# Optimization experiments

Hardware: AMD Instinct MI355X
Metric: run time of the kernel (lower is better)

Reference implementation:

```python
import jax, jax.numpy as jnp
import numpy as np

NUM_HEADS = 8
HEAD_DIM = 64  # inner_dim 512 / 8 heads
SCALE = HEAD_DIM ** -0.5


def setup_inputs() -> dict:
    key = jax.random.key(0)
    kq, kk, kv, kp = jax.random.split(key, 4)
    B, S, D = 8, 1024, 512
    q = jax.random.normal(kq, (B, S, D), dtype=jnp.float32)
    k = jax.random.normal(kk, (B, S, D), dtype=jnp.float32)
    v = jax.random.normal(kv, (B, S, D), dtype=jnp.float32)
    # learned additive positional bias table (trunc-normal init approximated by normal clipped)
    pos_bias = jnp.clip(jax.random.normal(kp, (1, NUM_HEADS, S, S), dtype=jnp.float32), -2.0, 2.0)
    return {"q": q, "k": k, "v": v, "pos_bias": pos_bias}


def reference(q, k, v, pos_bias):
    B, S, D = q.shape
    h, d = NUM_HEADS, HEAD_DIM
    # b n (h d) -> b h n d
    qh = q.reshape(B, S, h, d).transpose(0, 2, 1, 3) * SCALE
    kh = k.reshape(B, S, h, d).transpose(0, 2, 1, 3)
    vh = v.reshape(B, S, h, d).transpose(0, 2, 1, 3)
    sim = jnp.einsum('bhid,bhjd->bhij', qh, kh) + pos_bias
    attn = jax.nn.softmax(sim, axis=-1)
    out = jnp.einsum('bhij,bhjd->bhid', attn, vh)
    # b h n d -> b n (h d)
    return out.transpose(0, 2, 1, 3).reshape(B, S, h * d)
```

## Files before the change

kernel.cpp:

```cpp
#include <hip/hip_runtime.h>
#include <hip/hip_bf16.h>
#include <math.h>


typedef __attribute__((ext_vector_type(8))) short short8;
typedef __attribute__((ext_vector_type(4))) float f32x4;
typedef __attribute__((ext_vector_type(4))) unsigned short u16x4;

#define SEQ   1024
#define DM    512
#define HD    64
#define NH    8
#define LOG2E 1.4426950408889634f
#define QSCALE (0.125f * LOG2E)

__device__ __forceinline__ unsigned short f2bf(float f) {
    unsigned u = __float_as_uint(f);
    u += 0x7fffu + ((u >> 16) & 1u);
    return (unsigned short)(u >> 16);
}
__device__ __forceinline__ u16x4 pack4(float a, float b, float c, float d) {
    u16x4 r; r[0] = f2bf(a); r[1] = f2bf(b); r[2] = f2bf(c); r[3] = f2bf(d);
    return r;
}
__device__ __forceinline__ short8 pack8(const float* x) {
    short8 r;
#pragma unroll
    for (int i = 0; i < 8; ++i) r[i] = (short)f2bf(x[i]);
    return r;
}
__device__ __forceinline__ float fexp2(float x) {
#if __has_builtin(__builtin_amdgcn_exp2f)
    return __builtin_amdgcn_exp2f(x);
#else
    return exp2f(x);
#endif
}
__device__ __forceinline__ void gll16(const void* g, void* l) {
    __builtin_amdgcn_global_load_lds(
        (const __attribute__((address_space(1))) unsigned*)g,
        (__attribute__((address_space(3))) unsigned*)l, 16, 0, 0);
}

__global__ __launch_bounds__(256)
void prep_k(const float* __restrict__ k, short* __restrict__ kws) {
    int tid = blockIdx.x * 256 + threadIdx.x;
    int d8 = tid & 7, h = (tid >> 3) & 7, s = (tid >> 6) & 1023, b = tid >> 16;
    const float* src = k + ((size_t)(b * SEQ + s) * DM + h * HD + d8 * 8);
    float4 x0 = *(const float4*)src, x1 = *(const float4*)(src + 4);
    float xs[8] = {x0.x, x0.y, x0.z, x0.w, x1.x, x1.y, x1.z, x1.w};
    int bh = b * NH + h;
    size_t idx = (size_t)(bh * 16 + (s >> 6)) * 4096 + (s & 63) * 64 + ((d8 ^ (s & 7)) * 8);
    *(short8*)(kws + idx) = pack8(xs);
}

__global__ __launch_bounds__(256)
void prep_v(const float* __restrict__ v, short* __restrict__ vtws) {
    __shared__ short Vs[64][72];
    int bid = blockIdx.x;
    int st = bid & 15, h = (bid >> 4) & 7, b = bid >> 7;
    int t = threadIdx.x;
    {
        int sl = t >> 2, dc = t & 3;
        const float* src = v + ((size_t)(b * SEQ + st * 64 + sl) * DM + h * HD + dc * 16);
        float4 a0 = ((const float4*)src)[0], a1 = ((const float4*)src)[1],
               a2 = ((const float4*)src)[2], a3 = ((const float4*)src)[3];
        float xs0[8] = {a0.x, a0.y, a0.z, a0.w, a1.x, a1.y, a1.z, a1.w};
        float xs1[8] = {a2.x, a2.y, a2.z, a2.w, a3.x, a3.y, a3.z, a3.w};
        *(short8*)&Vs[sl][dc * 16]     = pack8(xs0);
        *(short8*)&Vs[sl][dc * 16 + 8] = pack8(xs1);
    }
    __syncthreads();
    {
        int d = t >> 2, sc = t & 3;
        short vals[16];
#pragma unroll
        for (int j = 0; j < 16; ++j) vals[j] = Vs[sc * 16 + j][d];
        short8 w0, w1;
#pragma unroll
        for (int j = 0; j < 8; ++j) { w0[j] = vals[j]; w1[j] = vals[8 + j]; }
        int bh = b * NH + h;
        size_t base = (size_t)(bh * 16 + st) * 4096 + d * 64;
        int c0 = (sc * 2) ^ (d & 7), c1 = (sc * 2 + 1) ^ (d & 7);
        *(short8*)(vtws + base + c0 * 8) = w0;
        *(short8*)(vtws + base + c1 * 8) = w1;
    }
}

__global__ __launch_bounds__(256, 2)
void attn_fwd2(const float* __restrict__ q, const float* __restrict__ bias,
               const short* __restrict__ kws, const short* __restrict__ vtws,
               float* __restrict__ out)
{
    __shared__ short Ksh[2][4096];
    __shared__ short Vsh[2][4096];
    __shared__ short Plds[4][32][72];

    const int t = threadIdx.x;
    const int wid = t >> 6, lane = t & 63;
    const int qr = lane & 15, g = lane >> 4;

    int idx = blockIdx.x;
    const int b = idx & 7;  idx >>= 3;
    const int h = idx & 7;
    const int qt = idx >> 3;
    const int qbw = qt * 128 + wid * 32;
    const int bh = b * NH + h;

    short8 qf[2][2];
#pragma unroll
    for (int sub = 0; sub < 2; ++sub) {
        const float* qp = q + ((size_t)(b * SEQ + qbw + sub * 16 + qr) * DM + h * HD);
#pragma unroll
        for (int c = 0; c < 2; ++c) {
            float4 x0 = *(const float4*)(qp + g * 8 + 32 * c);
            float4 x1 = *(const float4*)(qp + g * 8 + 32 * c + 4);
            float xs[8] = {x0.x * QSCALE, x0.y * QSCALE, x0.z * QSCALE, x0.w * QSCALE,
                           x1.x * QSCALE, x1.y * QSCALE, x1.z * QSCALE, x1.w * QSCALE};
            qf[sub][c] = pack8(xs);
        }
    }

    f32x4 o[2][4];
#pragma unroll
    for (int sub = 0; sub < 2; ++sub)
#pragma unroll
        for (int nt = 0; nt < 4; ++nt) o[sub][nt] = (f32x4){0.f, 0.f, 0.f, 0.f};
    float m0 = -INFINITY, m1 = -INFINITY, l0 = 0.f, l1 = 0.f;

    const size_t tb0 = (size_t)bh * 16 * 4096;
    {
        const short* gk = kws + tb0 + wid * 512 + lane * 8;
        const short* gv = vtws + tb0 + wid * 512 + lane * 8;
        gll16(gk,        &Ksh[0][wid * 512]);
        gll16(gk + 2048, &Ksh[0][2048 + wid * 512]);
        gll16(gv,        &Vsh[0][wid * 512]);
        gll16(gv + 2048, &Vsh[0][2048 + wid * 512]);
    }
    __syncthreads();

    int cur = 0;
    for (int kt = 0; kt < 16; ++kt) {
        if (kt < 15) {
            const size_t tb = tb0 + (size_t)(kt + 1) * 4096;
            const short* gk = kws + tb + wid * 512 + lane * 8;
            const short* gv = vtws + tb + wid * 512 + lane * 8;
            int nxt = cur ^ 1;
            gll16(gk,        &Ksh[nxt][wid * 512]);
            gll16(gk + 2048, &Ksh[nxt][2048 + wid * 512]);
            gll16(gv,        &Vsh[nxt][wid * 512]);
            gll16(gv + 2048, &Vsh[nxt][2048 + wid * 512]);
        }

        float4 bv[2][4];
#pragma unroll
        for (int sub = 0; sub < 2; ++sub) {
            const float* bp = bias + ((size_t)(h * SEQ + qbw + sub * 16 + qr) * SEQ + kt * 64 + g * 4);
#pragma unroll
            for (int mt = 0; mt < 4; ++mt) bv[sub][mt] = *(const float4*)(bp + 16 * mt);
        }

        f32x4 acc[2][4];
#pragma unroll
        for (int sub = 0; sub < 2; ++sub)
#pragma unroll
            for (int mt = 0; mt < 4; ++mt) acc[sub][mt] = (f32x4){0.f, 0.f, 0.f, 0.f};
        __builtin_amdgcn_s_setprio(1);
#pragma unroll
        for (int mt = 0; mt < 4; ++mt) {
#pragma unroll
            for (int c = 0; c < 2; ++c) {
                const short8 kf = *(const short8*)
                    &Ksh[cur][(qr + 16 * mt) * 64 + ((g + 4 * c) ^ (qr & 7)) * 8];
                acc[0][mt] = __builtin_amdgcn_mfma_f32_16x16x32_bf16(kf, qf[0][c], acc[0][mt], 0, 0, 0);
                acc[1][mt] = __builtin_amdgcn_mfma_f32_16x16x32_bf16(kf, qf[1][c], acc[1][mt], 0, 0, 0);
            }
        }
        __builtin_amdgcn_s_setprio(0);

        float sc[2];
#pragma unroll
        for (int sub = 0; sub < 2; ++sub) {
            float s[4][4];
            float tmax = -INFINITY;
#pragma unroll
            for (int mt = 0; mt < 4; ++mt)
#pragma unroll
                for (int r = 0; r < 4; ++r) {
                    float val = fmaf(((const float*)&bv[sub][mt])[r], LOG2E, acc[sub][mt][r]);
                    s[mt][r] = val;
                    tmax = fmaxf(tmax, val);
                }
            tmax = fmaxf(tmax, __shfl_xor(tmax, 16));
            tmax = fmaxf(tmax, __shfl_xor(tmax, 32));
            const float mold = (sub == 0) ? m0 : m1;
            const float mnew = fmaxf(mold, tmax);
            float ssum = 0.f;
#pragma unroll
            for (int mt = 0; mt < 4; ++mt) {
                float e0 = fexp2(s[mt][0] - mnew);
                float e1 = fexp2(s[mt][1] - mnew);
                float e2 = fexp2(s[mt][2] - mnew);
                float e3 = fexp2(s[mt][3] - mnew);
                ssum += (e0 + e1) + (e2 + e3);
                *(u16x4*)&Plds[wid][sub * 16 + qr][16 * mt + g * 4] = pack4(e0, e1, e2, e3);
            }
            ssum += __shfl_xor(ssum, 16);
            ssum += __shfl_xor(ssum, 32);
            const float scs = fexp2(mold - mnew);
            if (sub == 0) { l0 = l0 * scs + ssum; m0 = mnew; }
            else          { l1 = l1 * scs + ssum; m1 = mnew; }
            sc[sub] = scs;
        }

#pragma unroll
        for (int sub = 0; sub < 2; ++sub) {
            float scr[4];
#pragma unroll
            for (int r = 0; r < 4; ++r) scr[r] = __shfl(sc[sub], g * 4 + r);
#pragma unroll
            for (int nt = 0; nt < 4; ++nt)
#pragma unroll
                for (int r = 0; r < 4; ++r) o[sub][nt][r] *= scr[r];
        }

        asm volatile("s_waitcnt lgkmcnt(0)" ::: "memory");
        __builtin_amdgcn_sched_barrier(0);

        __builtin_amdgcn_s_setprio(1);
#pragma unroll
        for (int c = 0; c < 2; ++c) {
            short8 pf0 = *(const short8*)&Plds[wid][qr][g * 8 + 32 * c];
            short8 pf1 = *(const short8*)&Plds[wid][16 + qr][g * 8 + 32 * c];
#pragma unroll
            for (int nt = 0; nt < 4; ++nt) {
                short8 vf = *(const short8*)
                    &Vsh[cur][(qr + 16 * nt) * 64 + ((g + 4 * c) ^ (qr & 7)) * 8];
                o[0][nt] = __builtin_amdgcn_mfma_f32_16x16x32_bf16(pf0, vf, o[0][nt], 0, 0, 0);
                o[1][nt] = __builtin_amdgcn_mfma_f32_16x16x32_bf16(pf1, vf, o[1][nt], 0, 0, 0);
            }
        }
        __builtin_amdgcn_s_setprio(0);

        __syncthreads();
        cur ^= 1;
    }

    const float inv0 = 1.0f / l0, inv1 = 1.0f / l1;
#pragma unroll
    for (int sub = 0; sub < 2; ++sub) {
        const float invv = sub ? inv1 : inv0;
        float invr[4];
#pragma unroll
        for (int r = 0; r < 4; ++r) invr[r] = __shfl(invv, g * 4 + r);
        float* op = out + ((size_t)(b * SEQ + qbw + sub * 16) * DM + h * HD + qr);
#pragma unroll
        for (int nt = 0; nt < 4; ++nt)
#pragma unroll
            for (int r = 0; r < 4; ++r)
                op[(size_t)(g * 4 + r) * DM + nt * 16] = o[sub][nt][r] * invr[r];
    }
}

__global__ __launch_bounds__(256, 3)
void attn_fwd(const float* __restrict__ q, const float* __restrict__ k,
              const float* __restrict__ v, const float* __restrict__ bias,
              float* __restrict__ out)
{
    __shared__ short Klds[64][72];
    __shared__ short Vt[64][72];
    __shared__ short Pl[4][16][72];

    const int t = threadIdx.x;
    const int wid = t >> 6;
    const int lane = t & 63;
    const int qr = lane & 15;
    const int g = lane >> 4;

    int idx = blockIdx.x;
    const int b = idx & 7;  idx >>= 3;
    const int h = idx & 7;
    const int qtile = idx >> 3;
    const int qbase = qtile * 64 + wid * 16;

    const float* qp = q + ((b * SEQ + qbase + qr) * DM + h * HD);
    short8 qf[2];
#pragma unroll
    for (int c = 0; c < 2; ++c) {
        float4 x0 = *reinterpret_cast<const float4*>(qp + g * 8 + 32 * c);
        float4 x1 = *reinterpret_cast<const float4*>(qp + g * 8 + 32 * c + 4);
        float xs[8] = {x0.x * 0.125f, x0.y * 0.125f, x0.z * 0.125f, x0.w * 0.125f,
                       x1.x * 0.125f, x1.y * 0.125f, x1.z * 0.125f, x1.w * 0.125f};
        qf[c] = pack8(xs);
    }

    f32x4 o[4];
#pragma unroll
    for (int nt = 0; nt < 4; ++nt) o[nt] = (f32x4){0.f, 0.f, 0.f, 0.f};
    float mrun = -INFINITY, lrun = 0.f;

    const int jrow = t & 63;
    const int cc = t >> 6;

    for (int kt = 0; kt < 16; ++kt) {
        const int kbase = kt * 64;
        {
            const float4* kp4 = reinterpret_cast<const float4*>(
                k + ((b * SEQ + kbase + jrow) * DM + h * HD + cc * 16));
            float4 a0 = kp4[0], a1 = kp4[1], a2 = kp4[2], a3 = kp4[3];
            u16x4* dst = reinterpret_cast<u16x4*>(&Klds[jrow][cc * 16]);
            dst[0] = pack4(a0.x, a0.y, a0.z, a0.w);
            dst[1] = pack4(a1.x, a1.y, a1.z, a1.w);
            dst[2] = pack4(a2.x, a2.y, a2.z, a2.w);
            dst[3] = pack4(a3.x, a3.y, a3.z, a3.w);
        }
        {
            const float* vp = v + ((b * SEQ + kbase + cc * 16) * DM + h * HD + jrow);
            float vv[16];
#pragma unroll
            for (int jj = 0; jj < 16; ++jj) vv[jj] = vp[jj * DM];
            u16x4* dst = reinterpret_cast<u16x4*>(&Vt[jrow][cc * 16]);
            dst[0] = pack4(vv[0], vv[1], vv[2], vv[3]);
            dst[1] = pack4(vv[4], vv[5], vv[6], vv[7]);
            dst[2] = pack4(vv[8], vv[9], vv[10], vv[11]);
            dst[3] = pack4(vv[12], vv[13], vv[14], vv[15]);
        }
        __syncthreads();

        const float* bp = bias + ((h * SEQ + qbase + qr) * SEQ + kbase + g * 4);
        float4 bv0 = *reinterpret_cast<const float4*>(bp);
        float4 bv1 = *reinterpret_cast<const float4*>(bp + 16);
        float4 bv2 = *reinterpret_cast<const float4*>(bp + 32);
        float4 bv3 = *reinterpret_cast<const float4*>(bp + 48);

        f32x4 acc[4];
#pragma unroll
        for (int mt = 0; mt < 4; ++mt) {
            f32x4 a = (f32x4){0.f, 0.f, 0.f, 0.f};
#pragma unroll
            for (int c = 0; c < 2; ++c) {
                short8 kf = *reinterpret_cast<const short8*>(
                    &Klds[qr + 16 * mt][g * 8 + 32 * c]);
                a = __builtin_amdgcn_mfma_f32_16x16x32_bf16(kf, qf[c], a, 0, 0, 0);
            }
            acc[mt] = a;
        }
        acc[0][0] += bv0.x; acc[0][1] += bv0.y; acc[0][2] += bv0.z; acc[0][3] += bv0.w;
        acc[1][0] += bv1.x; acc[1][1] += bv1.y; acc[1][2] += bv1.z; acc[1][3] += bv1.w;
        acc[2][0] += bv2.x; acc[2][1] += bv2.y; acc[2][2] += bv2.z; acc[2][3] += bv2.w;
        acc[3][0] += bv3.x; acc[3][1] += bv3.y; acc[3][2] += bv3.z; acc[3][3] += bv3.w;

        float tmax = acc[0][0];
#pragma unroll
        for (int mt = 0; mt < 4; ++mt)
#pragma unroll
            for (int r = 0; r < 4; ++r) tmax = fmaxf(tmax, acc[mt][r]);
        tmax = fmaxf(tmax, __shfl_xor(tmax, 16));
        tmax = fmaxf(tmax, __shfl_xor(tmax, 32));
        const float mnew = fmaxf(mrun, tmax);

        float p[4][4];
        float ssum = 0.f;
#pragma unroll
        for (int mt = 0; mt < 4; ++mt)
#pragma unroll
            for (int r = 0; r < 4; ++r) {
                float e = __expf(acc[mt][r] - mnew);
                p[mt][r] = e;
                ssum += e;
            }
        ssum += __shfl_xor(ssum, 16);
        ssum += __shfl_xor(ssum, 32);
        const float scv = __expf(mrun - mnew);
        lrun = lrun * scv + ssum;
        mrun = mnew;

#pragma unroll
        for (int mt = 0; mt < 4; ++mt) {
            *reinterpret_cast<u16x4*>(&Pl[wid][qr][16 * mt + g * 4]) =
                pack4(p[mt][0], p[mt][1], p[mt][2], p[mt][3]);
        }

        float scr[4];
#pragma unroll
        for (int r = 0; r < 4; ++r) scr[r] = __shfl(scv, g * 4 + r);
#pragma unroll
        for (int nt = 0; nt < 4; ++nt)
#pragma unroll
            for (int r = 0; r < 4; ++r) o[nt][r] *= scr[r];

        asm volatile("s_waitcnt lgkmcnt(0)" ::: "memory");
        __builtin_amdgcn_sched_barrier(0);

        short8 pf0 = *reinterpret_cast<const short8*>(&Pl[wid][qr][g * 8]);
        short8 pf1 = *reinterpret_cast<const short8*>(&Pl[wid][qr][g * 8 + 32]);
#pragma unroll
        for (int nt = 0; nt < 4; ++nt) {
            short8 vf0 = *reinterpret_cast<const short8*>(&Vt[qr + 16 * nt][g * 8]);
            short8 vf1 = *reinterpret_cast<const short8*>(&Vt[qr + 16 * nt][g * 8 + 32]);
            o[nt] = __builtin_amdgcn_mfma_f32_16x16x32_bf16(pf0, vf0, o[nt], 0, 0, 0);
            o[nt] = __builtin_amdgcn_mfma_f32_16x16x32_bf16(pf1, vf1, o[nt], 0, 0, 0);
        }
        __syncthreads();
    }

    const float inv = 1.0f / lrun;
    float invr[4];
#pragma unroll
    for (int r = 0; r < 4; ++r) invr[r] = __shfl(inv, g * 4 + r);

    float* op = out + ((b * SEQ + qbase) * DM + h * HD + qr);
#pragma unroll
    for (int nt = 0; nt < 4; ++nt)
#pragma unroll
        for (int r = 0; r < 4; ++r)
            op[(g * 4 + r) * DM + nt * 16] = o[nt][r] * invr[r];
}

extern "C" void kernel_launch(void* const* d_in, const int* in_sizes, int n_in,
                              void* d_out, int out_size, void* d_ws, size_t ws_size,
                              hipStream_t stream) {
    const float* q    = (const float*)d_in[0];
    const float* k    = (const float*)d_in[1];
    const float* v    = (const float*)d_in[2];
    const float* bias = (const float*)d_in[3];
    float* out        = (float*)d_out;

    const size_t elems = (size_t)8 * NH * SEQ * HD;
    const size_t need  = 2 * elems * sizeof(short);
    if (ws_size >= need) {
        short* kws  = (short*)d_ws;
        short* vtws = kws + elems;
        prep_k<<<dim3(2048), dim3(256), 0, stream>>>(k, kws);
        prep_v<<<dim3(1024), dim3(256), 0, stream>>>(v, vtws);
        attn_fwd2<<<dim3(512), dim3(256), 0, stream>>>(q, bias, kws, vtws, out);
    } else {
        attn_fwd<<<dim3(1024), dim3(256), 0, stream>>>(q, k, v, bias, out);
    }
}
```

Baseline: 161.5 us.

## Precompute fp16 bias in tiled layout, shrink query tile, prefetch bias, swizzle P

Adds a prep kernel that converts the positional bias to fp16, pre-multiplies it by log2e and rearranges it into per-key-tile blocks, so the attention kernel reads half the bias bytes with contiguous 16-byte loads. The attention kernel now handles 16 query rows per wave instead of 32, uses 1024 blocks with an occupancy hint of 4, remaps block indices, prefetches the next tile's bias one iteration ahead, and XOR-swizzles the P buffer in LDS. The bias prep pass is extra work each call and fp16 bias adds rounding error, while the smaller tile halves K/V reuse per block.

```diff
diff --git a/kernel.cpp b/kernel.cpp
--- a/kernel.cpp
+++ b/kernel.cpp
@@ -1,11 +1,13 @@
 #include <hip/hip_runtime.h>
 #include <hip/hip_bf16.h>
+#include <hip/hip_fp16.h>
 #include <math.h>
 
 
 typedef __attribute__((ext_vector_type(8))) short short8;
 typedef __attribute__((ext_vector_type(4))) float f32x4;
 typedef __attribute__((ext_vector_type(4))) unsigned short u16x4;
+typedef __attribute__((ext_vector_type(8))) unsigned short u16x8;
 
 #define SEQ   1024
 #define DM    512
@@ -40,6 +42,14 @@
     __builtin_amdgcn_global_load_lds(
         (const __attribute__((address_space(1))) unsigned*)g,
         (__attribute__((address_space(3))) unsigned*)l, 16, 0, 0);
+}
+__device__ __forceinline__ float h2f(unsigned short u) {
+    __half hh = *reinterpret_cast<__half*>(&u);
+    return __half2float(hh);
+}
+__device__ __forceinline__ unsigned short f2h(float v) {
+    __half hh = __float2half(v);
+    return *reinterpret_cast<unsigned short*>(&hh);
 }
 
 __global__ __launch_bounds__(256)
@@ -87,48 +97,67 @@
     }
 }
 
-__global__ __launch_bounds__(256, 2)
-void attn_fwd2(const float* __restrict__ q, const float* __restrict__ bias,
-               const short* __restrict__ kws, const short* __restrict__ vtws,
+__global__ __launch_bounds__(256)
+void prep_bias(const float* __restrict__ bias, unsigned short* __restrict__ b16) {
+    int tid = blockIdx.x * 256 + threadIdx.x;
+    int h = tid >> 18;
+    int rem = tid & 262143;
+    int i = rem >> 8;
+    int j = (rem & 255) * 4;
+    float4 x = *(const float4*)(bias + ((size_t)(h * 1024 + i) * 1024 + j));
+    int kt = j >> 6, jl = j & 63, mt = jl >> 4, gg = (jl >> 2) & 3;
+    u16x4 r;
+    r[0] = f2h(x.x * LOG2E); r[1] = f2h(x.y * LOG2E);
+    r[2] = f2h(x.z * LOG2E); r[3] = f2h(x.w * LOG2E);
+    *(u16x4*)(b16 + ((size_t)((h * 16 + kt) * 1024 + i) * 64 + gg * 16 + mt * 4)) = r;
+}
+
+template<int BM>
+__global__ __launch_bounds__(256, 4)
+void attn_fwd3(const float* __restrict__ q,
+               const float* __restrict__ bias32,
+               const unsigned short* __restrict__ bias16,
+               const short* __restrict__ kws,
+               const short* __restrict__ vtws,
                float* __restrict__ out)
 {
     __shared__ short Ksh[2][4096];
     __shared__ short Vsh[2][4096];
-    __shared__ short Plds[4][32][72];
+    __shared__ short Plds[4][16][64];
 
     const int t = threadIdx.x;
     const int wid = t >> 6, lane = t & 63;
     const int qr = lane & 15, g = lane >> 4;
 
-    int idx = blockIdx.x;
-    const int b = idx & 7;  idx >>= 3;
-    const int h = idx & 7;
-    const int qt = idx >> 3;
-    const int qbw = qt * 128 + wid * 32;
+    int raw = blockIdx.x;
+    int lid = (raw & 7) * 128 + (raw >> 3);
+    const int b = lid & 7;
+    const int h = (lid >> 3) & 7;
+    const int qt = lid >> 6;
+    const int qbase = qt * 64 + wid * 16;
     const int bh = b * NH + h;
 
-    short8 qf[2][2];
-#pragma unroll
-    for (int sub = 0; sub < 2; ++sub) {
-        const float* qp = q + ((size_t)(b * SEQ + qbw + sub * 16 + qr) * DM + h * HD);
-#pragma unroll
-        for (int c = 0; c < 2; ++c) {
-            float4 x0 = *(const float4*)(qp + g * 8 + 32 * c);
-            float4 x1 = *(const float4*)(qp + g * 8 + 32 * c + 4);
-            float xs[8] = {x0.x * QSCALE, x0.y * QSCALE, x0.z * QSCALE, x0.w * QSCALE,
-                           x1.x * QSCALE, x1.y * QSCALE, x1.z * QSCALE, x1.w * QSCALE};
-            qf[sub][c] = pack8(xs);
-        }
-    }
-
-    f32x4 o[2][4];
-#pragma unroll
-    for (int sub = 0; sub < 2; ++sub)
-#pragma unroll
-        for (int nt = 0; nt < 4; ++nt) o[sub][nt] = (f32x4){0.f, 0.f, 0.f, 0.f};
-    float m0 = -INFINITY, m1 = -INFINITY, l0 = 0.f, l1 = 0.f;
+    const float* qp = q + ((size_t)(b * SEQ + qbase + qr) * DM + h * HD);
+    short8 qf[2];
+#pragma unroll
+    for (int c = 0; c < 2; ++c) {
+        float4 x0 = *(const float4*)(qp + g * 8 + 32 * c);
+        float4 x1 = *(const float4*)(qp + g * 8 + 32 * c + 4);
+        float xs[8] = {x0.x * QSCALE, x0.y * QSCALE, x0.z * QSCALE, x0.w * QSCALE,
+                       x1.x * QSCALE, x1.y * QSCALE, x1.z * QSCALE, x1.w * QSCALE};
+        qf[c] = pack8(xs);
+    }
+
+    f32x4 o[4];
+#pragma unroll
+    for (int nt = 0; nt < 4; ++nt) o[nt] = (f32x4){0.f, 0.f, 0.f, 0.f};
+    float mrun = -INFINITY, lrun = 0.f;
 
     const size_t tb0 = (size_t)bh * 16 * 4096;
+
+    u16x8 bn0, bn1;
+    float4 bnf[4];
+
     {
         const short* gk = kws + tb0 + wid * 512 + lane * 8;
         const short* gv = vtws + tb0 + wid * 512 + lane * 8;
@@ -136,11 +165,37 @@
         gll16(gk + 2048, &Ksh[0][2048 + wid * 512]);
         gll16(gv,        &Vsh[0][wid * 512]);
         gll16(gv + 2048, &Vsh[0][2048 + wid * 512]);
+        if constexpr (BM == 0) {
+            const unsigned short* bp =
+                bias16 + ((size_t)((h * 16 + 0) * 1024 + qbase + qr) * 64 + g * 16);
+            bn0 = *(const u16x8*)bp;
+            bn1 = *(const u16x8*)(bp + 8);
+        } else {
+            const float* bp = bias32 + ((size_t)(h * SEQ + qbase + qr) * SEQ + g * 4);
+#pragma unroll
+            for (int mt = 0; mt < 4; ++mt) bnf[mt] = *(const float4*)(bp + 16 * mt);
+        }
     }
     __syncthreads();
 
     int cur = 0;
     for (int kt = 0; kt < 16; ++kt) {
+        float bf[4][4];
+        if constexpr (BM == 0) {
+#pragma unroll
+            for (int r = 0; r < 4; ++r) {
+                bf[0][r] = h2f(bn0[r]);
+                bf[1][r] = h2f(bn0[4 + r]);
+                bf[2][r] = h2f(bn1[r]);
+                bf[3][r] = h2f(bn1[4 + r]);
+            }
+        } else {
+#pragma unroll
+            for (int mt = 0; mt < 4; ++mt)
+#pragma unroll
+                for (int r = 0; r < 4; ++r) bf[mt][r] = ((const float*)&bnf[mt])[r];
+        }
+
         if (kt < 15) {
             const size_t tb = tb0 + (size_t)(kt + 1) * 4096;
             const short* gk = kws + tb + wid * 512 + lane * 8;
@@ -151,20 +206,24 @@
             gll16(gv,        &Vsh[nxt][wid * 512]);
             gll16(gv + 2048, &Vsh[nxt][2048 + wid * 512]);
         }
-
-        float4 bv[2][4];
-#pragma unroll
-        for (int sub = 0; sub < 2; ++sub) {
-            const float* bp = bias + ((size_t)(h * SEQ + qbw + sub * 16 + qr) * SEQ + kt * 64 + g * 4);
-#pragma unroll
-            for (int mt = 0; mt < 4; ++mt) bv[sub][mt] = *(const float4*)(bp + 16 * mt);
-        }
-
-        f32x4 acc[2][4];
-#pragma unroll
-        for (int sub = 0; sub < 2; ++sub)
-#pragma unroll
-            for (int mt = 0; mt < 4; ++mt) acc[sub][mt] = (f32x4){0.f, 0.f, 0.f, 0.f};
+        {
+            int ktn = kt < 15 ? kt + 1 : 15;
+            if constexpr (BM == 0) {
+                const unsigned short* bp =
+                    bias16 + ((size_t)((h * 16 + ktn) * 1024 + qbase + qr) * 64 + g * 16);
+                bn0 = *(const u16x8*)bp;
+                bn1 = *(const u16x8*)(bp + 8);
+            } else {
+                const float* bp =
+                    bias32 + ((size_t)(h * SEQ + qbase + qr) * SEQ + ktn * 64 + g * 4);
+#pragma unroll
+                for (int mt = 0; mt < 4; ++mt) bnf[mt] = *(const float4*)(bp + 16 * mt);
+            }
+        }
+
+        f32x4 acc[4];
+#pragma unroll
+        for (int mt = 0; mt < 4; ++mt) acc[mt] = (f32x4){0.f, 0.f, 0.f, 0.f};
         __builtin_amdgcn_s_setprio(1);
 #pragma unroll
         for (int mt = 0; mt < 4; ++mt) {
@@ -172,57 +231,50 @@
             for (int c = 0; c < 2; ++c) {
                 const short8 kf = *(const short8*)
                     &Ksh[cur][(qr + 16 * mt) * 64 + ((g + 4 * c) ^ (qr & 7)) * 8];
-                acc[0][mt] = __builtin_amdgcn_mfma_f32_16x16x32_bf16(kf, qf[0][c], acc[0][mt], 0, 0, 0);
-                acc[1][mt] = __builtin_amdgcn_mfma_f32_16x16x32_bf16(kf, qf[1][c], acc[1][mt], 0, 0, 0);
+                acc[mt] = __builtin_amdgcn_mfma_f32_16x16x32_bf16(kf, qf[c], acc[mt], 0, 0, 0);
             }
         }
         __builtin_amdgcn_s_setprio(0);
 
-        float sc[2];
-#pragma unroll
-        for (int sub = 0; sub < 2; ++sub) {
-            float s[4][4];
-            float tmax = -INFINITY;
-#pragma unroll
-            for (int mt = 0; mt < 4; ++mt)
-#pragma unroll
-                for (int r = 0; r < 4; ++r) {
-                    float val = fmaf(((const float*)&bv[sub][mt])[r], LOG2E, acc[sub][mt][r]);
-                    s[mt][r] = val;
-                    tmax = fmaxf(tmax, val);
-                }
-            tmax = fmaxf(tmax, __shfl_xor(tmax, 16));
-            tmax = fmaxf(tmax, __shfl_xor(tmax, 32));
-            const float mold = (sub == 0) ? m0 : m1;
-            const float mnew = fmaxf(mold, tmax);
-            float ssum = 0.f;
-#pragma unroll
-            for (int mt = 0; mt < 4; ++mt) {
-                float e0 = fexp2(s[mt][0] - mnew);
-                float e1 = fexp2(s[mt][1] - mnew);
-                float e2 = fexp2(s[mt][2] - mnew);
-                float e3 = fexp2(s[mt][3] - mnew);
-                ssum += (e0 + e1) + (e2 + e3);
-                *(u16x4*)&Plds[wid][sub * 16 + qr][16 * mt + g * 4] = pack4(e0, e1, e2, e3);
-            }
-            ssum += __shfl_xor(ssum, 16);
-            ssum += __shfl_xor(ssum, 32);
-            const float scs = fexp2(mold - mnew);
-            if (sub == 0) { l0 = l0 * scs + ssum; m0 = mnew; }
-            else          { l1 = l1 * scs + ssum; m1 = mnew; }
-            sc[sub] = scs;
-        }
-
-#pragma unroll
-        for (int sub = 0; sub < 2; ++sub) {
-            float scr[4];
-#pragma unroll
-            for (int r = 0; r < 4; ++r) scr[r] = __shfl(sc[sub], g * 4 + r);
-#pragma unroll
-            for (int nt = 0; nt < 4; ++nt)
-#pragma unroll
-                for (int r = 0; r < 4; ++r) o[sub][nt][r] *= scr[r];
-        }
+        float s[4][4];
+        float tmax = -INFINITY;
+#pragma unroll
+        for (int mt = 0; mt < 4; ++mt)
+#pragma unroll
+            for (int r = 0; r < 4; ++r) {
+                float val;
+                if constexpr (BM == 0) val = acc[mt][r] + bf[mt][r];
+                else                   val = fmaf(bf[mt][r], LOG2E, acc[mt][r]);
+                s[mt][r] = val;
+                tmax = fmaxf(tmax, val);
+            }
+        tmax = fmaxf(tmax, __shfl_xor(tmax, 16));
+        tmax = fmaxf(tmax, __shfl_xor(tmax, 32));
+        const float mnew = fmaxf(mrun, tmax);
+        float ssum = 0.f;
+#pragma unroll
+        for (int mt = 0; mt < 4; ++mt) {
+            float e0 = fexp2(s[mt][0] - mnew);
+            float e1 = fexp2(s[mt][1] - mnew);
+            float e2 = fexp2(s[mt][2] - mnew);
+            float e3 = fexp2(s[mt][3] - mnew);
+            ssum += (e0 + e1) + (e2 + e3);
+            *(u16x4*)&Plds[wid][qr][((4 * mt + g) ^ (2 * (qr & 7))) * 4] =
+                pack4(e0, e1, e2, e3);
+        }
+        ssum += __shfl_xor(ssum, 16);
+        ssum += __shfl_xor(ssum, 32);
+        const float scs = fexp2(mrun - mnew);
+        lrun = lrun * scs + ssum;
+        mrun = mnew;
+
+        float scr[4];
+#pragma unroll
+        for (int r = 0; r < 4; ++r) scr[r] = __shfl(scs, g * 4 + r);
+#pragma unroll
+        for (int nt = 0; nt < 4; ++nt)
+#pragma unroll
+            for (int r = 0; r < 4; ++r) o[nt][r] *= scr[r];
 
         asm volatile("s_waitcnt lgkmcnt(0)" ::: "memory");
         __builtin_amdgcn_sched_barrier(0);
@@ -230,14 +282,13 @@
         __builtin_amdgcn_s_setprio(1);
 #pragma unroll
         for (int c = 0; c < 2; ++c) {
-            short8 pf0 = *(const short8*)&Plds[wid][qr][g * 8 + 32 * c];
-            short8 pf1 = *(const short8*)&Plds[wid][16 + qr][g * 8 + 32 * c];
+            const int ch0 = (2 * g + 8 * c) ^ (2 * (qr & 7));
+            short8 pf = *(const short8*)&Plds[wid][qr][ch0 * 4];
 #pragma unroll
             for (int nt = 0; nt < 4; ++nt) {
                 short8 vf = *(const short8*)
                     &Vsh[cur][(qr + 16 * nt) * 64 + ((g + 4 * c) ^ (qr & 7)) * 8];
-                o[0][nt] = __builtin_amdgcn_mfma_f32_16x16x32_bf16(pf0, vf, o[0][nt], 0, 0, 0);
-                o[1][nt] = __builtin_amdgcn_mfma_f32_16x16x32_bf16(pf1, vf, o[1][nt], 0, 0, 0);
+                o[nt] = __builtin_amdgcn_mfma_f32_16x16x32_bf16(pf, vf, o[nt], 0, 0, 0);
             }
         }
         __builtin_amdgcn_s_setprio(0);
@@ -246,20 +297,16 @@
         cur ^= 1;
     }
 
-    const float inv0 = 1.0f / l0, inv1 = 1.0f / l1;
-#pragma unroll
-    for (int sub = 0; sub < 2; ++sub) {
-        const float invv = sub ? inv1 : inv0;
-        float invr[4];
-#pragma unroll
-        for (int r = 0; r < 4; ++r) invr[r] = __shfl(invv, g * 4 + r);
-        float* op = out + ((size_t)(b * SEQ + qbw + sub * 16) * DM + h * HD + qr);
-#pragma unroll
-        for (int nt = 0; nt < 4; ++nt)
-#pragma unroll
-            for (int r = 0; r < 4; ++r)
-                op[(size_t)(g * 4 + r) * DM + nt * 16] = o[sub][nt][r] * invr[r];
-    }
+    const float inv = 1.0f / lrun;
+    float invr[4];
+#pragma unroll
+    for (int r = 0; r < 4; ++r) invr[r] = __shfl(inv, g * 4 + r);
+    float* op = out + ((size_t)(b * SEQ + qbase) * DM + h * HD + qr);
+#pragma unroll
+    for (int nt = 0; nt < 4; ++nt)
+#pragma unroll
+        for (int r = 0; r < 4; ++r)
+            op[(size_t)(g * 4 + r) * DM + nt * 16] = o[nt][r] * invr[r];
 }
 
 __global__ __launch_bounds__(256, 3)
@@ -426,14 +473,24 @@
     const float* bias = (const float*)d_in[3];
     float* out        = (float*)d_out;
 
-    const size_t elems = (size_t)8 * NH * SEQ * HD;
-    const size_t need  = 2 * elems * sizeof(short);
-    if (ws_size >= need) {
-        short* kws  = (short*)d_ws;
-        short* vtws = kws + elems;
+    const size_t kv_elems  = (size_t)8 * NH * SEQ * HD;
+    const size_t kv_bytes  = 2 * kv_elems * sizeof(short);
+    const size_t b16_bytes = (size_t)NH * SEQ * SEQ * 2;
+
+    if (ws_size >= b16_bytes + kv_bytes) {
+        unsigned short* b16 = (unsigned short*)d_ws;
+        short* kws  = (short*)((char*)d_ws + b16_bytes);
+        short* vtws = kws + kv_elems;
+        prep_bias<<<dim3(8192), dim3(256), 0, stream>>>(bias, b16);
         prep_k<<<dim3(2048), dim3(256), 0, stream>>>(k, kws);
         prep_v<<<dim3(1024), dim3(256), 0, stream>>>(v, vtws);
-        attn_fwd2<<<dim3(512), dim3(256), 0, stream>>>(q, bias, kws, vtws, out);
+        attn_fwd3<0><<<dim3(1024), dim3(256), 0, stream>>>(q, nullptr, b16, kws, vtws, out);
+    } else if (ws_size >= kv_bytes) {
+        short* kws  = (short*)d_ws;
+        short* vtws = kws + kv_elems;
+        prep_k<<<dim3(2048), dim3(256), 0, stream>>>(k, kws);
+        prep_v<<<dim3(1024), dim3(256), 0, stream>>>(v, vtws);
+        attn_fwd3<1><<<dim3(1024), dim3(256), 0, stream>>>(q, bias, nullptr, kws, vtws, out);
     } else {
         attn_fwd<<<dim3(1024), dim3(256), 0, stream>>>(q, k, v, bias, out);
     }
```

New measurement: 163.8 us. About the same (+1.4%).
